# Optimization experiments

Measured on AMD Instinct MI355X. Metric: run time of the kernel, lower is better.

## Reference

```python
import jax, jax.numpy as jnp
import numpy as np

BS, SL, NN, NE = 8, 100, 200, 600
C = 110; CP1 = C + 1
D = 128          # node_embed_dim
DC = 64          # concept_embed_dim
H = 256          # lstm hidden
VOCAB = 50000
NPROB = 1000
FEAT = 2 + CP1 + DC  # LSTM input dim = 177


def setup_inputs() -> dict:
    key = jax.random.key(0)
    ks = jax.random.split(key, 24)
    f32 = jnp.float32
    p_id = jax.random.randint(ks[0], (BS, SL), 0, NPROB)
    c_id = jax.random.bernoulli(ks[1], 0.1, (BS, SL, CP1)).astype(f32)
    node_id = jax.random.randint(ks[2], (BS, SL, NN), 0, VOCAB)
    edge = jax.random.randint(ks[3], (BS, SL, 2, NE), 0, NN)
    edge_type = jax.random.randint(ks[4], (BS, SL, NE), 0, 8)
    target_c = jax.random.bernoulli(ks[5], 0.05, (BS, SL, CP1)).astype(f32)
    target_c = target_c.at[:, :, 0].set(1.0)  # every step has >=1 target concept
    result = jax.random.bernoulli(ks[6], 0.5, (BS * SL, 1)).astype(f32)
    c_embed = jax.random.bernoulli(ks[7], 0.1, (BS, SL, CP1)).astype(f32)
    cur_result = jax.random.normal(ks[8], (BS, SL, 2), f32)
    # parameters
    node_embed_w = jax.random.normal(ks[9], (VOCAB, D), f32) * 0.02
    edge_embed_w = (jax.random.normal(ks[10], (8, D), f32) * 0.02).at[0].set(0.0)  # padding_idx=0
    ggnn_w = jax.random.normal(ks[11], (4, D, D), f32) * 0.05
    gru_w_ih = jax.random.normal(ks[12], (3 * D, D), f32) * 0.05
    gru_w_hh = jax.random.normal(ks[13], (3 * D, D), f32) * 0.05
    gru_b_ih = jnp.zeros((3 * D,), f32)
    gru_b_hh = jnp.zeros((3 * D,), f32)
    transdim_w = jax.random.normal(ks[14], (DC, D), f32) * 0.05
    concept_embedding = jax.random.normal(ks[15], (CP1, DC), f32) * 0.05
    lstm_w_ih = jax.random.normal(ks[16], (4 * H, FEAT), f32) * 0.05
    lstm_w_hh = jax.random.normal(ks[17], (4 * H, H), f32) * 0.05
    lstm_b_ih = jnp.zeros((4 * H,), f32)
    lstm_b_hh = jnp.zeros((4 * H,), f32)
    pred_w = jax.random.normal(ks[18], (CP1, H), f32) * 0.05
    pred_b = jnp.zeros((CP1,), f32)
    return dict(p_id=p_id, c_id=c_id, node_id=node_id, edge=edge, edge_type=edge_type,
                target_c=target_c, result=result, c_embed=c_embed, cur_result=cur_result,
                node_embed_w=node_embed_w, edge_embed_w=edge_embed_w, ggnn_w=ggnn_w,
                gru_w_ih=gru_w_ih, gru_w_hh=gru_w_hh, gru_b_ih=gru_b_ih, gru_b_hh=gru_b_hh,
                transdim_w=transdim_w, concept_embedding=concept_embedding,
                lstm_w_ih=lstm_w_ih, lstm_w_hh=lstm_w_hh, lstm_b_ih=lstm_b_ih,
                lstm_b_hh=lstm_b_hh, pred_w=pred_w, pred_b=pred_b)


def _forward(p_id, c_id, node_id, edge, edge_type, target_c, result, c_embed, cur_result,
             node_embed_w, edge_embed_w, ggnn_w, gru_w_ih, gru_w_hh, gru_b_ih, gru_b_hh,
             transdim_w, concept_embedding, lstm_w_ih, lstm_w_hh, lstm_b_ih, lstm_b_hh,
             pred_w, pred_b):
    bs, sl = p_id.shape
    N = node_id.shape[2]
    G = bs * sl  # all graphs batched (replaces torch per-sample python loop)
    x = node_embed_w[node_id].reshape(G, N, -1)                       # [G,N,D]
    ew = edge_embed_w[edge_type].mean(-1).reshape(G, -1, 1)           # [G,E,1]
    e = edge.reshape(G, 2, -1)
    src, dst = e[:, 0], e[:, 1]                                       # [G,E]
    flat_dst = (dst + jnp.arange(G)[:, None] * N).reshape(-1)
    d = x.shape[-1]
    # GatedGraphConv, 4 layers: m = x @ W_l, sum-aggregate edge_weight*m[src] at dst, GRUCell update
    for l in range(4):
        m = jnp.einsum('gnd,de->gne', x, ggnn_w[l])
        gathered = jnp.take_along_axis(m, src[:, :, None], axis=1)    # [G,E,D]
        msg = (ew * gathered).reshape(-1, d)
        agg = jax.ops.segment_sum(msg, flat_dst, num_segments=G * N).reshape(G, N, d)
        gi = agg @ gru_w_ih.T + gru_b_ih
        gh = x @ gru_w_hh.T + gru_b_hh
        i_r, i_z, i_n = jnp.split(gi, 3, axis=-1)
        h_r, h_z, h_n = jnp.split(gh, 3, axis=-1)
        r = jax.nn.sigmoid(i_r + h_r)
        z = jax.nn.sigmoid(i_z + h_z)
        n = jnp.tanh(i_n + r * h_n)
        x = (1.0 - z) * n + z * x
    # transdim (node_embed_dim != concept_embed_dim)
    ggnn = jnp.einsum('gnd,cd->gnc', x, transdim_w)                   # [G,N,DC]
    # concept-node attention
    ce = c_embed.reshape(G, -1, 1)                                    # [G,C+1,1]
    query = ce * concept_embedding[None]                              # [G,C+1,DC]
    attn_w = jax.nn.softmax(jnp.einsum('gcd,gnd->gcn', query, ggnn), axis=2)
    attn = jnp.einsum('gcn,gnd->gcd', attn_w, ggnn) * ce
    num = jnp.sum(c_id, axis=2).reshape(G, 1)
    num = jnp.where(num == 0, 1.0, num)
    attn_out = (jnp.sum(attn, axis=1) / num).reshape(bs, sl, -1)
    # LSTM (1 layer, batch_first)
    lstm_in = jnp.concatenate([c_embed, attn_out, cur_result], axis=2)
    hdim = pred_w.shape[1]
    def step(carry, xt):
        h, c = carry
        gates = xt @ lstm_w_ih.T + lstm_b_ih + h @ lstm_w_hh.T + lstm_b_hh
        i, f, g, o = jnp.split(gates, 4, axis=-1)
        c = jax.nn.sigmoid(f) * c + jax.nn.sigmoid(i) * jnp.tanh(g)
        h = jax.nn.sigmoid(o) * jnp.tanh(c)
        return (h, c), h
    init = (jnp.zeros((bs, hdim), lstm_in.dtype), jnp.zeros((bs, hdim), lstm_in.dtype))
    _, hs = jax.lax.scan(step, init, jnp.swapaxes(lstm_in, 0, 1))
    lstm_out = jnp.swapaxes(hs, 0, 1).reshape(G, hdim)
    # prediction + masked BCE-with-logits
    pred = lstm_out @ pred_w.T + pred_b                               # [G,C+1]
    tc = target_c.reshape(G, -1)
    pred1 = jnp.sum(pred * tc, axis=1)
    nc = jnp.sum(tc, axis=1)
    mask = nc > 0
    fp = pred1 / jnp.where(mask, nc, 1.0)
    ft = result.reshape(-1)
    bce = jnp.maximum(fp, 0.0) - fp * ft + jnp.log1p(jnp.exp(-jnp.abs(fp)))
    mf = mask.astype(fp.dtype)
    loss = jnp.sum(bce * mf) / jnp.maximum(jnp.sum(mf), 1.0)
    return loss, jax.nn.sigmoid(fp), ft


def reference(p_id, c_id, node_id, edge, edge_type, target_c, result, c_embed, cur_result,
              node_embed_w, edge_embed_w, ggnn_w, gru_w_ih, gru_w_hh, gru_b_ih, gru_b_hh,
              transdim_w, concept_embedding, lstm_w_ih, lstm_w_hh, lstm_b_ih, lstm_b_hh,
              pred_w, pred_b):
    return _forward(p_id, c_id, node_id, edge, edge_type, target_c, result, c_embed, cur_result,
                    node_embed_w, edge_embed_w, ggnn_w, gru_w_ih, gru_w_hh, gru_b_ih, gru_b_hh,
                    transdim_w, concept_embedding, lstm_w_ih, lstm_w_hh, lstm_b_ih, lstm_b_hh,
                    pred_w, pred_b)
```

## Files before the change

### kernel.cpp

```cpp
#include <hip/hip_runtime.h>
#include <math.h>

static const int BSZ   = 8;
static const int SLN   = 100;
static const int NNODE = 200;
static const int NEDGE = 600;
static const int CP1N  = 111;
static const int DIM   = 128;
static const int DCN   = 64;
static const int HID   = 256;
static const int FEATN = 177;
static const int GN    = 800;
static const int MROW  = 160000;

typedef unsigned short u16;
typedef u16    u16x8  __attribute__((ext_vector_type(8)));
typedef __bf16 bf16x8 __attribute__((ext_vector_type(8)));
typedef __bf16 bf16x2 __attribute__((ext_vector_type(2)));
typedef float  f32x16 __attribute__((ext_vector_type(16)));

#if defined(__has_builtin)
# if __has_builtin(__builtin_amdgcn_fdot2_f32_bf16)
#  define HAVE_FDOT2 1
# else
// ... 103 lines not shown
    } else if (idx < 172032){
        int t = idx - 163840;
        twb[t] = f2bf(tw[t]);
    }
}

__global__ void __launch_bounds__(256)
k_build_csr(const int* __restrict__ edge, const int* __restrict__ etype,
            const float* __restrict__ eembed,
            int* __restrict__ csr_src, float* __restrict__ csr_w, int* __restrict__ csr_off){
    int g = blockIdx.x; int tid = threadIdx.x;
    __shared__ float tmean[8];
    __shared__ float tpart[8][32];
    __shared__ int cnt[NNODE];
    __shared__ int offs[NNODE+1];
    __shared__ int cur[NNODE];
    {
        int ty = tid >> 5, lane = tid & 31;
        float s = 0.f;
        for (int i = lane; i < DIM; i += 32) s += eembed[ty*DIM + i];
        tpart[ty][lane] = s;
    }
    for (int i = tid; i < NNODE; i += 256) cnt[i] = 0;
    __syncthreads();
    if (tid < 8){
        float s = 0.f;
        for (int i = 0; i < 32; i++) s += tpart[tid][i];
        tmean[tid] = s / (float)DIM;
    }
    for (int e = tid; e < NEDGE; e += 256){
        int dst = edge[((size_t)g*2+1)*NEDGE + e];
        atomicAdd(&cnt[dst], 1);
    }
    __syncthreads();
    if (tid == 0){
        int run = 0;
        for (int i = 0; i < NNODE; i++){ offs[i] = run; run += cnt[i]; }
        offs[NNODE] = run;
    }
    __syncthreads();
    for (int i = tid; i < NNODE; i += 256) cur[i] = offs[i];
    for (int i = tid; i < NNODE+1; i += 256) csr_off[(size_t)g*(NNODE+1)+i] = offs[i];
    __syncthreads();
    for (int e = tid; e < NEDGE; e += 256){
        int dst = edge[((size_t)g*2+1)*NEDGE + e];
        int src = edge[((size_t)g*2+0)*NEDGE + e];
        float w = tmean[etype[(size_t)g*NEDGE + e]];
        int pos = atomicAdd(&cur[dst], 1);
        csr_src[(size_t)g*NEDGE + pos] = src;
        csr_w [(size_t)g*NEDGE + pos] = w;
    }
}

__global__ void __launch_bounds__(256)
k_mm_scatter(const u16* __restrict__ xb, const u16* __restrict__ gwTb_l,
             const int* __restrict__ csr_src, const float* __restrict__ csr_w,
             const int* __restrict__ csr_off, u16* __restrict__ aggb,
             const float4* __restrict__ emb, const int* __restrict__ nid, int first){
    __shared__ u16 smem[224*128];
    __shared__ int   e_src[NEDGE];
    __shared__ float e_w[NEDGE];
    __shared__ int   offs_s[NNODE+1];
    int g = blockIdx.x;
    int tid = threadIdx.x;
    u16x8* afrag = (u16x8*)smem;
    if (first){
        for (int c = tid; c < 3584; c += 256){
            int row = c >> 4, kc8 = c & 15;
            u16x8 v = {};
            if (row < NNODE) v = pack_emb(emb, nid[(size_t)g*NNODE + row], kc8);
            afrag[afrag_slot(row, kc8)] = v;
        }
    } else {
        const u16x8* xg = (const u16x8*)(xb + (size_t)g*NNODE*DIM);
        for (int c = tid; c < 3584; c += 256){
            int row = c >> 4, kc8 = c & 15;
            u16x8 v = {};
            if (row < NNODE) v = xg[row*16 + kc8];
            afrag[afrag_slot(row, kc8)] = v;
        }
    }
    {
        const int*   srcp = csr_src + (size_t)g*NEDGE;
        const float* wp   = csr_w   + (size_t)g*NEDGE;
        const int*   off  = csr_off + (size_t)g*(NNODE+1);
        for (int i = tid; i < NEDGE; i += 256){ e_src[i] = srcp[i]; e_w[i] = wp[i]; }
        for (int i = tid; i <= NNODE; i += 256) offs_s[i] = off[i];
    }
    __syncthreads();
    int w = tid >> 6, lane = tid & 63;
    int nbase = w*32;
    int m = lane & 31, kh = lane >> 5;
    f32x16 acc[7];
    #pragma unroll
    for (int t = 0; t < 7; t++) acc[t] = (f32x16)0.f;
    const u16x8* bp = (const u16x8*)gwTb_l;
    int nrow = nbase + m;
    #pragma unroll
    for (int kc = 0; kc < 8; kc++){
        u16x8 b = bp[nrow*16 + kc*2 + kh];
        #pragma unroll
        for (int mt = 0; mt < 7; mt++){
            u16x8 a = afrag[(mt*8 + kc)*64 + (lane ^ kc)];
            acc[mt] = __builtin_amdgcn_mfma_f32_32x32x16_bf16(
                __builtin_bit_cast(bf16x8, a), __builtin_bit_cast(bf16x8, b), acc[mt], 0, 0, 0);
        }
    }
    __syncthreads();
    #pragma unroll
    for (int mt = 0; mt < 7; mt++){
        #pragma unroll
        for (int r = 0; r < 16; r++){
            int row = mt*32 + (r&3) + 8*(r>>2) + 4*kh;
            int col = nbase + m;
            smem[row*128 + col] = f2bf(acc[mt][r]);
        }
    }
    __syncthreads();
    const unsigned* m32 = (const unsigned*)smem;
    int j2 = tid & 63, rg = tid >> 6;
    unsigned* aggout = (unsigned*)(aggb + (size_t)g*NNODE*DIM);
    for (int i = 0; i < 50; i++){
        int n = rg*50 + i;
        int b0 = offs_s[n], e0 = offs_s[n+1];
        float a0 = 0.f, a1 = 0.f;
        for (int p = b0; p < e0; p++){
            unsigned mv = m32[e_src[p]*64 + j2];
            float w_ = e_w[p];
            a0 += w_ * bf2f((u16)(mv & 0xffffu));
            a1 += w_ * bf2f((u16)(mv >> 16));
        }
        aggout[(size_t)n*64 + j2] = (unsigned)f2bf(a0) | ((unsigned)f2bf(a1) << 16);
    }
}

__global__ void __launch_bounds__(512, 2)
k_gru_mfma(u16* __restrict__ xb, const u16* __restrict__ aggb,
           const u16* __restrict__ wihb, const u16* __restrict__ whhb,
           const float* __restrict__ bih, const float* __restrict__ bhh,
           const float4* __restrict__ emb, const int* __restrict__ nid, int first){
    __shared__ u16x8 afragA[2048];
    __shared__ u16x8 afragX[2048];
    int tid = threadIdx.x;
    long r0 = (long)blockIdx.x * 128;
    const u16x8* aggp = (const u16x8*)aggb;
    if (first){
        for (int c = tid; c < 2048; c += 512){
            int row = c >> 4, kc8 = c & 15;
            afragX[afrag_slot(row, kc8)] = pack_emb(emb, nid[r0 + row], kc8);
        }
        for (int c = tid; c < 2048; c += 512){
            int row = c >> 4, kc8 = c & 15;
            afragA[afrag_slot(row, kc8)] = aggp[(r0 + row)*16 + kc8];
        }
    } else {
        const u16x8* xbp = (const u16x8*)xb;
        for (int c = tid; c < 4096; c += 512){
            int mat = c >> 11, cc = c & 2047;
            int row = cc >> 4, kc8 = cc & 15;
            u16x8 v = (mat ? xbp : aggp)[(r0 + row)*16 + kc8];
            (mat ? afragX : afragA)[afrag_slot(row, kc8)] = v;
        }
    }
    __syncthreads();
    int w = tid >> 6, lane = tid & 63;
    int mtg = w >> 2;
    int cb  = (w & 3) * 32;
    f32x16 acc0[6], acc1[6];
    #pragma unroll
    for (int t = 0; t < 6; t++){ acc0[t] = (f32x16)0.f; acc1[t] = (f32x16)0.f; }
    const u16x8* bi = (const u16x8*)wihb;
    const u16x8* bh = (const u16x8*)whhb;
    int kh = lane >> 5;
    int ncol = cb + (lane & 31);
    #pragma unroll
    for (int kc = 0; kc < 8; kc++){
        int lx = lane ^ kc;
        u16x8 aA0 = afragA[((2*mtg+0)*8 + kc)*64 + lx];
        u16x8 aA1 = afragA[((2*mtg+1)*8 + kc)*64 + lx];
        u16x8 aX0 = afragX[((2*mtg+0)*8 + kc)*64 + lx];
        u16x8 aX1 = afragX[((2*mtg+1)*8 + kc)*64 + lx];
        #pragma unroll
        for (int g3 = 0; g3 < 3; g3++){
            int n = g3*128 + ncol;
            u16x8 b1 = bi[n*16 + kc*2 + kh];
            u16x8 b2 = bh[n*16 + kc*2 + kh];
            acc0[g3]   = __builtin_amdgcn_mfma_f32_32x32x16_bf16(
                __builtin_bit_cast(bf16x8, aA0), __builtin_bit_cast(bf16x8, b1), acc0[g3], 0,0,0);
            acc1[g3]   = __builtin_amdgcn_mfma_f32_32x32x16_bf16(
                __builtin_bit_cast(bf16x8, aA1), __builtin_bit_cast(bf16x8, b1), acc1[g3], 0,0,0);
            acc0[3+g3] = __builtin_amdgcn_mfma_f32_32x32x16_bf16(
                __builtin_bit_cast(bf16x8, aX0), __builtin_bit_cast(bf16x8, b2), acc0[3+g3], 0,0,0);
            acc1[3+g3] = __builtin_amdgcn_mfma_f32_32x32x16_bf16(
                __builtin_bit_cast(bf16x8, aX1), __builtin_bit_cast(bf16x8, b2), acc1[3+g3], 0,0,0);
        }
    }
    int col = cb + (lane & 31);
    float bir = bih[col], biz = bih[col+128], bin = bih[col+256];
    float bhr = bhh[col], bhz = bhh[col+128], bhn = bhh[col+256];
    int kc8c = col >> 3, elc = col & 7;
    #pragma unroll
    for (int mt2 = 0; mt2 < 2; mt2++){
        const f32x16* ac = mt2 ? acc1 : acc0;
        #pragma unroll
        for (int r = 0; r < 16; r++){
            int row = mtg*64 + mt2*32 + (r&3) + 8*(r>>2) + 4*kh;
            u16x8 xv = afragX[afrag_slot(row, kc8c)];
            float xo = bf2f(((const u16*)&xv)[elc]);
            float rr  = sigf(ac[0][r] + bir + ac[3][r] + bhr);
            float zz  = sigf(ac[1][r] + biz + ac[4][r] + bhz);
            float nn_ = tanh_f(ac[2][r] + bin + rr*(ac[5][r] + bhn));
            float xn  = (1.f - zz)*nn_ + zz*xo;
            xb[(size_t)(r0 + row)*DIM + col] = f2bf(xn);
        }
    }
}

__global__ void __launch_bounds__(256)
k_attention(const u16* __restrict__ xb, const u16* __restrict__ twb,
            const float* __restrict__ cemb, const float* __restrict__ cid,
            const float* __restrict__ conc, const float* __restrict__ curres,
            float* __restrict__ lstm_in){
    int g = blockIdx.x; int tid = threadIdx.x;
    int lane = tid & 63, wv = tid >> 6;
    __shared__ __align__(16) unsigned char smem_raw[57344];
    __shared__ float ce_s[CP1N];
    __shared__ float sc4[4][256];
    __shared__ float wredA[4][4];
    __shared__ float wredB[4][4];
    __shared__ float part4[4][4][DCN];
    __shared__ float oacc[DCN];
    __shared__ float num_s;
    __shared__ int actv[CP1N];
    __shared__ int nact_s;
    u16x8* afrag = (u16x8*)smem_raw;
    float* gg    = (float*)smem_raw;
    const u16x8* xg = (const u16x8*)(xb + (size_t)g*NNODE*DIM);
    for (int c = tid; c < 3584; c += 256){
        int row = c >> 4, kc8 = c & 15;
        u16x8 v = {};
        if (row < NNODE) v = xg[row*16 + kc8];
        afrag[afrag_slot(row, kc8)] = v;
    }
    if (tid == 0) nact_s = 0;
    if (tid < CP1N) ce_s[tid] = cemb[(size_t)g*CP1N + tid];
    if (tid < DCN) oacc[tid] = 0.f;
    {
        float v = (tid < CP1N) ? cid[(size_t)g*CP1N + tid] : 0.f;
        #pragma unroll
        for (int m2 = 32; m2; m2 >>= 1) v += __shfl_xor(v, m2);
        if (lane == 0) wredA[wv][0] = v;
    }
    __syncthreads();
    if (tid == 0){
        float nm = wredA[0][0]+wredA[1][0]+wredA[2][0]+wredA[3][0];
        num_s = (nm == 0.f) ? 1.f : nm;
    }
    if (tid < CP1N && ce_s[tid] != 0.f){
        int p = atomicAdd(&nact_s, 1);
        actv[p] = tid;
    }
    {
        int ct = wv & 1, rh = wv >> 1;
        int tb = rh ? 4 : 0;
        int ntile = rh ? 3 : 4;
        int m = lane & 31, kh = lane >> 5;
        f32x16 acc[4];
        #pragma unroll
        for (int t = 0; t < 4; t++) acc[t] = (f32x16)0.f;
        const u16x8* tp = (const u16x8*)twb;
        #pragma unroll
        for (int kc = 0; kc < 8; kc++){
            u16x8 b = tp[(ct*32 + m)*16 + kc*2 + kh];
            #pragma unroll
            for (int t = 0; t < 4; t++){
                if (t < ntile){
                    u16x8 a = afrag[((tb+t)*8 + kc)*64 + (lane ^ kc)];
                    acc[t] = __builtin_amdgcn_mfma_f32_32x32x16_bf16(
                        __builtin_bit_cast(bf16x8, a), __builtin_bit_cast(bf16x8, b), acc[t], 0,0,0);
                }
            }
        }
        __syncthreads();
        #pragma unroll
        for (int t = 0; t < 4; t++){
            if (t < ntile){
                #pragma unroll
                for (int r = 0; r < 16; r++){
                    int row = (tb+t)*32 + (r&3) + 8*(r>>2) + 4*kh;
                    int col = ct*32 + m;
                    if (row < NNODE) gg[row*65 + col] = acc[t][r];
                }
            }
        }
    }
    __syncthreads();
    int nact = nact_s;
    for (int ci = 0; ci < nact; ci += 4){
        int i0 = actv[ci];
        int i1 = actv[(ci+1 < nact) ? ci+1 : nact-1];
        int i2 = actv[(ci+2 < nact) ? ci+2 : nact-1];
        int i3 = actv[(ci+3 < nact) ? ci+3 : nact-1];
        float ce0 = ce_s[i0], ce1 = ce_s[i1], ce2 = ce_s[i2], ce3 = ce_s[i3];
        const float* q0 = conc + i0*DCN;
        const float* q1 = conc + i1*DCN;
        const float* q2 = conc + i2*DCN;
        const float* q3 = conc + i3*DCN;
        float s0=-1e30f, s1=-1e30f, s2=-1e30f, s3=-1e30f;
        if (tid < NNODE){
            float a0=0.f,a1=0.f,a2=0.f,a3=0.f;
            const float* gr_ = &gg[tid*65];
            #pragma unroll 8
            for (int d = 0; d < DCN; d++){
                float gv = gr_[d];
                a0 += q0[d]*gv; a1 += q1[d]*gv; a2 += q2[d]*gv; a3 += q3[d]*gv;
            }
            s0 = ce0*a0; s1 = ce1*a1; s2 = ce2*a2; s3 = ce3*a3;
        }
        float m0=s0, m1=s1, m2=s2, m3=s3;
        #pragma unroll
        for (int mk = 32; mk; mk >>= 1){
            m0 = fmaxf(m0, __shfl_xor(m0, mk));
            m1 = fmaxf(m1, __shfl_xor(m1, mk));
            m2 = fmaxf(m2, __shfl_xor(m2, mk));
            m3 = fmaxf(m3, __shfl_xor(m3, mk));
        }
        if (lane == 0){ wredA[wv][0]=m0; wredA[wv][1]=m1; wredA[wv][2]=m2; wredA[wv][3]=m3; }
        __syncthreads();
        float mx0 = fmaxf(fmaxf(wredA[0][0],wredA[1][0]), fmaxf(wredA[2][0],wredA[3][0]));
        float mx1 = fmaxf(fmaxf(wredA[0][1],wredA[1][1]), fmaxf(wredA[2][1],wredA[3][1]));
        float mx2 = fmaxf(fmaxf(wredA[0][2],wredA[1][2]), fmaxf(wredA[2][2],wredA[3][2]));
        float mx3 = fmaxf(fmaxf(wredA[0][3],wredA[1][3]), fmaxf(wredA[2][3],wredA[3][3]));
        float e0 = (tid < NNODE) ? fexp2(LOG2E*(s0-mx0)) : 0.f;
        float e1 = (tid < NNODE) ? fexp2(LOG2E*(s1-mx1)) : 0.f;
        float e2 = (tid < NNODE) ? fexp2(LOG2E*(s2-mx2)) : 0.f;
        float e3 = (tid < NNODE) ? fexp2(LOG2E*(s3-mx3)) : 0.f;
        sc4[0][tid]=e0; sc4[1][tid]=e1; sc4[2][tid]=e2; sc4[3][tid]=e3;
        float u0=e0,u1=e1,u2=e2,u3=e3;
        #pragma unroll
        for (int mk = 32; mk; mk >>= 1){
            u0 += __shfl_xor(u0, mk);
            u1 += __shfl_xor(u1, mk);
            u2 += __shfl_xor(u2, mk);
            u3 += __shfl_xor(u3, mk);
        }
        if (lane == 0){ wredB[wv][0]=u0; wredB[wv][1]=u1; wredB[wv][2]=u2; wredB[wv][3]=u3; }
        __syncthreads();
        float inv0 = ce0 / (wredB[0][0]+wredB[1][0]+wredB[2][0]+wredB[3][0]);
        float inv1 = (ci+1 < nact) ? ce1 / (wredB[0][1]+wredB[1][1]+wredB[2][1]+wredB[3][1]) : 0.f;
        float inv2 = (ci+2 < nact) ? ce2 / (wredB[0][2]+wredB[1][2]+wredB[2][2]+wredB[3][2]) : 0.f;
        float inv3 = (ci+3 < nact) ? ce3 / (wredB[0][3]+wredB[1][3]+wredB[2][3]+wredB[3][3]) : 0.f;
        float pa0=0.f, pa1=0.f, pa2=0.f, pa3=0.f;
        for (int n = wv; n < NNODE; n += 4){
            float gv = gg[n*65 + lane];
            pa0 += sc4[0][n]*gv; pa1 += sc4[1][n]*gv;
            pa2 += sc4[2][n]*gv; pa3 += sc4[3][n]*gv;
        }
        part4[wv][0][lane]=pa0; part4[wv][1][lane]=pa1;
        part4[wv][2][lane]=pa2; part4[wv][3][lane]=pa3;
        __syncthreads();
        if (tid < DCN){
            float t0 = part4[0][0][tid]+part4[1][0][tid]+part4[2][0][tid]+part4[3][0][tid];
            float t1 = part4[0][1][tid]+part4[1][1][tid]+part4[2][1][tid]+part4[3][1][tid];
            float t2 = part4[0][2][tid]+part4[1][2][tid]+part4[2][2][tid]+part4[3][2][tid];
            float t3 = part4[0][3][tid]+part4[1][3][tid]+part4[2][3][tid]+part4[3][3][tid];
            oacc[tid] += inv0*t0 + inv1*t1 + inv2*t2 + inv3*t3;
        }
    }
    __syncthreads();
    if (tid < FEATN){
        float v;
        if      (tid < CP1N)       v = ce_s[tid];
        else if (tid < CP1N+DCN)   v = oacc[tid-CP1N] / num_s;
        else                       v = curres[(size_t)g*2 + (tid-CP1N-DCN)];
        lstm_in[(size_t)g*FEATN + tid] = v;
    }
}

__global__ void __launch_bounds__(256)
k_gi(const float* __restrict__ lstm_in, const float* __restrict__ wihT,
     const float* __restrict__ bih, const float* __restrict__ bhh, float* __restrict__ gi){
    int rb = blockIdx.x;
    int jb = blockIdx.y;
    int tid = threadIdx.x;
    __shared__ float in_s[8][FEATN];
    for (int i = tid; i < 8*FEATN; i += 256){ int r = i/FEATN, k = i%FEATN; in_s[r][k] = lstm_in[((size_t)rb*8+r)*FEATN + k]; }
    __syncthreads();
    int j = jb*256 + tid;
    float acc[8];
    #pragma unroll
    for (int i = 0; i < 8; i++) acc[i] = 0.f;
    for (int k = 0; k < FEATN; k++){
        float w = wihT[(size_t)k*1024 + j];
        #pragma unroll
        for (int i = 0; i < 8; i++) acc[i] += in_s[i][k] * w;
    }
    float b = bih[j] + bhh[j];
    #pragma unroll
    for (int i = 0; i < 8; i++) gi[((size_t)rb*8+i)*1024 + j] = acc[i] + b;
}

static const int WREG = 104;
static const int WL4  = 6;

__global__ void __launch_bounds__(1024)
__attribute__((amdgpu_waves_per_eu(4,4)))
k_lstm(const float* __restrict__ gi, const unsigned* __restrict__ whhP, float* __restrict__ out){
    int b = blockIdx.x; int tid = threadIdx.x;
    __shared__ uint4 ldsw4[WL4][1024];
    __shared__ float gates[1024];
    __shared__ __align__(8) u16 h16[HID];
    unsigned wreg[WREG];
    #pragma unroll
    for (int i = 0; i < WREG; i++) wreg[i] = whhP[(size_t)i*1024 + tid];
    #pragma unroll
    for (int q = 0; q < WL4; q++){
        uint4 v;
        v.x = whhP[(size_t)(WREG + 4*q + 0)*1024 + tid];
        v.y = whhP[(size_t)(WREG + 4*q + 1)*1024 + tid];
        v.z = whhP[(size_t)(WREG + 4*q + 2)*1024 + tid];
        v.w = whhP[(size_t)(WREG + 4*q + 3)*1024 + tid];
        ldsw4[q][tid] = v;
    }
    if (tid < 128) ((unsigned*)h16)[tid] = 0u;
    float c_reg = 0.f;
    int lane = tid & 63;
    __syncthreads();
    float giv = gi[(size_t)b*SLN*1024 + tid];
// ... 75 lines not shown
        __syncthreads();
    }
    if (tid == 0){
        float nc = redn[0];
        bool mask = nc > 0.f;
        float fp = redv[0] / (mask ? nc : 1.f);
        float ft = result[row];
        float bce = fmaxf(fp, 0.f) - fp*ft + log1pf(expf(-fabsf(fp)));
        out[1 + row]      = 1.f/(1.f + expf(-fp));
        out[1 + GN + row] = ft;
        if (mask){ atomicAdd(&lacc[0], bce); atomicAdd(&lacc[1], 1.f); }
    }
}

__global__ void k_loss_final(const float* __restrict__ lacc, float* __restrict__ out){
    out[0] = lacc[0] / fmaxf(lacc[1], 1.f);
}

extern "C" void kernel_launch(void* const* d_in, const int* in_sizes, int n_in,
                              void* d_out, int out_size, void* d_ws, size_t ws_size,
                              hipStream_t stream) {
    const float* c_id        = (const float*)d_in[1];
    const int*   node_id     = (const int*)  d_in[2];
    const int*   edge        = (const int*)  d_in[3];
    const int*   etype       = (const int*)  d_in[4];
    const float* target_c    = (const float*)d_in[5];
    const float* result      = (const float*)d_in[6];
    const float* c_embed     = (const float*)d_in[7];
    const float* cur_result  = (const float*)d_in[8];
    const float* node_emb_w  = (const float*)d_in[9];
    const float* edge_emb_w  = (const float*)d_in[10];
    const float* ggnn_w      = (const float*)d_in[11];
    const float* gru_w_ih    = (const float*)d_in[12];
    const float* gru_w_hh    = (const float*)d_in[13];
    const float* gru_b_ih    = (const float*)d_in[14];
    const float* gru_b_hh    = (const float*)d_in[15];
    const float* transdim_w  = (const float*)d_in[16];
    const float* concept     = (const float*)d_in[17];
    const float* lstm_w_ih   = (const float*)d_in[18];
    const float* lstm_w_hh   = (const float*)d_in[19];
    const float* lstm_b_ih   = (const float*)d_in[20];
    const float* lstm_b_hh   = (const float*)d_in[21];
    const float* pred_w      = (const float*)d_in[22];
    const float* pred_b      = (const float*)d_in[23];
    float* out = (float*)d_out;

    char* ws = (char*)d_ws;
    size_t off = 0;
    auto alloc = [&](size_t bytes) -> void* {
        void* p = ws + off;
        off += (bytes + 255) & ~(size_t)255;
        return p;
    };
    u16*      xb       = (u16*)     alloc((size_t)MROW*DIM*2);
    u16*      aggb     = (u16*)     alloc((size_t)MROW*DIM*2);
    int*      csr_src  = (int*)     alloc((size_t)GN*NEDGE*4);
    float*    csr_w    = (float*)   alloc((size_t)GN*NEDGE*4);
    int*      csr_off  = (int*)     alloc((size_t)GN*(NNODE+1)*4);
    float*    lstm_in  = (float*)   alloc((size_t)GN*FEATN*4);
    float*    gi       = (float*)   alloc((size_t)GN*1024*4);
    unsigned* whhP     = (unsigned*)alloc((size_t)128*1024*4);
    float*    wihT     = (float*)   alloc((size_t)FEATN*1024*4);
    float*    lstm_out = (float*)   alloc((size_t)GN*HID*4);
    u16*      wihb     = (u16*)     alloc((size_t)384*128*2);
    u16*      whhb     = (u16*)     alloc((size_t)384*128*2);
    u16*      gwTb     = (u16*)     alloc((size_t)4*128*128*2);
    u16*      twb      = (u16*)     alloc((size_t)DCN*DIM*2);
    float*    lacc     = (float*)   alloc(256);

    hipMemsetAsync(lacc, 0, 8, stream);
    {
        int total = 128*1024 + FEATN*1024;
        k_transpose_w<<<(total + 255)/256, 256, 0, stream>>>(lstm_w_hh, lstm_w_ih, whhP, wihT);
    }
    k_convert_w<<<672, 256, 0, stream>>>(gru_w_ih, gru_w_hh, ggnn_w, transdim_w, wihb, whhb, gwTb, twb);
    k_build_csr<<<GN, 256, 0, stream>>>(edge, etype, edge_emb_w, csr_src, csr_w, csr_off);
    for (int l = 0; l < 4; l++){
        k_mm_scatter<<<GN, 256, 0, stream>>>(xb, gwTb + (size_t)l*DIM*DIM,
                                             csr_src, csr_w, csr_off, aggb,
                                             (const float4*)node_emb_w, node_id, l == 0);
        k_gru_mfma<<<MROW/128, 512, 0, stream>>>(xb, aggb, wihb, whhb, gru_b_ih, gru_b_hh,
                                                 (const float4*)node_emb_w, node_id, l == 0);
    }
    k_attention<<<GN, 256, 0, stream>>>(xb, twb, c_embed, c_id, concept, cur_result, lstm_in);
    k_gi<<<dim3(100, 4), 256, 0, stream>>>(lstm_in, wihT, lstm_b_ih, lstm_b_hh, gi);
    k_lstm<<<BSZ, 1024, 0, stream>>>(gi, whhP, lstm_out);
    k_final<<<GN, 128, 0, stream>>>(lstm_out, pred_w, pred_b, target_c, result, out, lacc);
    k_loss_final<<<1, 1, 0, stream>>>(lacc, out);
}
```

Measured before the change: 1.123 ms.

## Fuse all GGNN layers, GRU updates and attention into one per-graph kernel

Replaces the four pairs of message-matmul/scatter and GRU kernels plus the attention kernel with a single 512-thread kernel per graph. Node states and aggregated messages stay in LDS across all four layers, which removes the global xb/aggb round trips and eight kernel launches. The message matrix is built in two 64-column halves so it fits in scratch. In exchange, occupancy drops sharply because of the large LDS footprint, and the GRU GEMM now runs at only 800 blocks with some idle waves for the 7-tile split.

```diff
diff --git a/kernel.cpp b/kernel.cpp
--- a/kernel.cpp
+++ b/kernel.cpp
@@ -179,230 +179,183 @@
     }
 }
 
-__global__ void __launch_bounds__(256)
-k_mm_scatter(const u16* __restrict__ xb, const u16* __restrict__ gwTb_l,
-             const int* __restrict__ csr_src, const float* __restrict__ csr_w,
-             const int* __restrict__ csr_off, u16* __restrict__ aggb,
-             const float4* __restrict__ emb, const int* __restrict__ nid, int first){
-    __shared__ u16 smem[224*128];
+__global__ void __launch_bounds__(512)
+k_ggnn(const float4* __restrict__ emb, const int* __restrict__ nid,
+       const u16* __restrict__ gwTb, const u16* __restrict__ wihb,
+       const u16* __restrict__ whhb, const float* __restrict__ bih,
+       const float* __restrict__ bhh,
+       const int* __restrict__ csr_src, const float* __restrict__ csr_w,
+       const int* __restrict__ csr_off, const u16* __restrict__ twb,
+       const float* __restrict__ cemb, const float* __restrict__ cid,
+       const float* __restrict__ conc, const float* __restrict__ curres,
+       float* __restrict__ lstm_in){
+    __shared__ u16x8 Xf[3584];
+    __shared__ u16x8 Af[3584];
+    __shared__ __align__(16) unsigned char scratch[28672];
     __shared__ int   e_src[NEDGE];
     __shared__ float e_w[NEDGE];
     __shared__ int   offs_s[NNODE+1];
-    int g = blockIdx.x;
-    int tid = threadIdx.x;
-    u16x8* afrag = (u16x8*)smem;
-    if (first){
-        for (int c = tid; c < 3584; c += 256){
-            int row = c >> 4, kc8 = c & 15;
-            u16x8 v = {};
-            if (row < NNODE) v = pack_emb(emb, nid[(size_t)g*NNODE + row], kc8);
-            afrag[afrag_slot(row, kc8)] = v;
-        }
-    } else {
-        const u16x8* xg = (const u16x8*)(xb + (size_t)g*NNODE*DIM);
-        for (int c = tid; c < 3584; c += 256){
-            int row = c >> 4, kc8 = c & 15;
-            u16x8 v = {};
-            if (row < NNODE) v = xg[row*16 + kc8];
-            afrag[afrag_slot(row, kc8)] = v;
-        }
+    __shared__ float ce_s[CP1N];
+    __shared__ float redw[8];
+    __shared__ float num_s;
+    __shared__ int   actv[CP1N];
+    __shared__ int   nact_s;
+
+    int g = blockIdx.x; int tid = threadIdx.x;
+    int lane = tid & 63, wv = tid >> 6;
+    int m = lane & 31, kh = lane >> 5;
+
+    for (int c = tid; c < 3584; c += 512){
+        int row = c >> 4, kc8 = c & 15;
+        u16x8 v = {};
+        if (row < NNODE) v = pack_emb(emb, nid[(size_t)g*NNODE + row], kc8);
+        Xf[afrag_slot(row, kc8)] = v;
     }
     {
         const int*   srcp = csr_src + (size_t)g*NEDGE;
         const float* wp   = csr_w   + (size_t)g*NEDGE;
         const int*   off  = csr_off + (size_t)g*(NNODE+1);
-        for (int i = tid; i < NEDGE; i += 256){ e_src[i] = srcp[i]; e_w[i] = wp[i]; }
-        for (int i = tid; i <= NNODE; i += 256) offs_s[i] = off[i];
-    }
-    __syncthreads();
-    int w = tid >> 6, lane = tid & 63;
-    int nbase = w*32;
-    int m = lane & 31, kh = lane >> 5;
-    f32x16 acc[7];
-    #pragma unroll
-    for (int t = 0; t < 7; t++) acc[t] = (f32x16)0.f;
-    const u16x8* bp = (const u16x8*)gwTb_l;
-    int nrow = nbase + m;
-    #pragma unroll
-    for (int kc = 0; kc < 8; kc++){
-        u16x8 b = bp[nrow*16 + kc*2 + kh];
-        #pragma unroll
-        for (int mt = 0; mt < 7; mt++){
-            u16x8 a = afrag[(mt*8 + kc)*64 + (lane ^ kc)];
-            acc[mt] = __builtin_amdgcn_mfma_f32_32x32x16_bf16(
-                __builtin_bit_cast(bf16x8, a), __builtin_bit_cast(bf16x8, b), acc[mt], 0, 0, 0);
-        }
-    }
-    __syncthreads();
-    #pragma unroll
-    for (int mt = 0; mt < 7; mt++){
-        #pragma unroll
-        for (int r = 0; r < 16; r++){
-            int row = mt*32 + (r&3) + 8*(r>>2) + 4*kh;
-            int col = nbase + m;
-            smem[row*128 + col] = f2bf(acc[mt][r]);
-        }
-    }
-    __syncthreads();
-    const unsigned* m32 = (const unsigned*)smem;
-    int j2 = tid & 63, rg = tid >> 6;
-    unsigned* aggout = (unsigned*)(aggb + (size_t)g*NNODE*DIM);
-    for (int i = 0; i < 50; i++){
-        int n = rg*50 + i;
-        int b0 = offs_s[n], e0 = offs_s[n+1];
-        float a0 = 0.f, a1 = 0.f;
-        for (int p = b0; p < e0; p++){
-            unsigned mv = m32[e_src[p]*64 + j2];
-            float w_ = e_w[p];
-            a0 += w_ * bf2f((u16)(mv & 0xffffu));
-            a1 += w_ * bf2f((u16)(mv >> 16));
-        }
-        aggout[(size_t)n*64 + j2] = (unsigned)f2bf(a0) | ((unsigned)f2bf(a1) << 16);
-    }
-}
-
-__global__ void __launch_bounds__(512, 2)
-k_gru_mfma(u16* __restrict__ xb, const u16* __restrict__ aggb,
-           const u16* __restrict__ wihb, const u16* __restrict__ whhb,
-           const float* __restrict__ bih, const float* __restrict__ bhh,
-           const float4* __restrict__ emb, const int* __restrict__ nid, int first){
-    __shared__ u16x8 afragA[2048];
-    __shared__ u16x8 afragX[2048];
-    int tid = threadIdx.x;
-    long r0 = (long)blockIdx.x * 128;
-    const u16x8* aggp = (const u16x8*)aggb;
-    if (first){
-        for (int c = tid; c < 2048; c += 512){
-            int row = c >> 4, kc8 = c & 15;
-            afragX[afrag_slot(row, kc8)] = pack_emb(emb, nid[r0 + row], kc8);
-        }
-        for (int c = tid; c < 2048; c += 512){
-            int row = c >> 4, kc8 = c & 15;
-            afragA[afrag_slot(row, kc8)] = aggp[(r0 + row)*16 + kc8];
-        }
-    } else {
-        const u16x8* xbp = (const u16x8*)xb;
-        for (int c = tid; c < 4096; c += 512){
-            int mat = c >> 11, cc = c & 2047;
-            int row = cc >> 4, kc8 = cc & 15;
-            u16x8 v = (mat ? xbp : aggp)[(r0 + row)*16 + kc8];
-            (mat ? afragX : afragA)[afrag_slot(row, kc8)] = v;
-        }
-    }
-    __syncthreads();
-    int w = tid >> 6, lane = tid & 63;
-    int mtg = w >> 2;
-    int cb  = (w & 3) * 32;
-    f32x16 acc0[6], acc1[6];
-    #pragma unroll
-    for (int t = 0; t < 6; t++){ acc0[t] = (f32x16)0.f; acc1[t] = (f32x16)0.f; }
-    const u16x8* bi = (const u16x8*)wihb;
-    const u16x8* bh = (const u16x8*)whhb;
-    int kh = lane >> 5;
-    int ncol = cb + (lane & 31);
-    #pragma unroll
-    for (int kc = 0; kc < 8; kc++){
-        int lx = lane ^ kc;
-        u16x8 aA0 = afragA[((2*mtg+0)*8 + kc)*64 + lx];
-        u16x8 aA1 = afragA[((2*mtg+1)*8 + kc)*64 + lx];
-        u16x8 aX0 = afragX[((2*mtg+0)*8 + kc)*64 + lx];
-        u16x8 aX1 = afragX[((2*mtg+1)*8 + kc)*64 + lx];
-        #pragma unroll
-        for (int g3 = 0; g3 < 3; g3++){
-            int n = g3*128 + ncol;
-            u16x8 b1 = bi[n*16 + kc*2 + kh];
-            u16x8 b2 = bh[n*16 + kc*2 + kh];
-            acc0[g3]   = __builtin_amdgcn_mfma_f32_32x32x16_bf16(
-                __builtin_bit_cast(bf16x8, aA0), __builtin_bit_cast(bf16x8, b1), acc0[g3], 0,0,0);
-            acc1[g3]   = __builtin_amdgcn_mfma_f32_32x32x16_bf16(
-                __builtin_bit_cast(bf16x8, aA1), __builtin_bit_cast(bf16x8, b1), acc1[g3], 0,0,0);
-            acc0[3+g3] = __builtin_amdgcn_mfma_f32_32x32x16_bf16(
-                __builtin_bit_cast(bf16x8, aX0), __builtin_bit_cast(bf16x8, b2), acc0[3+g3], 0,0,0);
-            acc1[3+g3] = __builtin_amdgcn_mfma_f32_32x32x16_bf16(
-                __builtin_bit_cast(bf16x8, aX1), __builtin_bit_cast(bf16x8, b2), acc1[3+g3], 0,0,0);
-        }
-    }
-    int col = cb + (lane & 31);
-    float bir = bih[col], biz = bih[col+128], bin = bih[col+256];
-    float bhr = bhh[col], bhz = bhh[col+128], bhn = bhh[col+256];
-    int kc8c = col >> 3, elc = col & 7;
-    #pragma unroll
-    for (int mt2 = 0; mt2 < 2; mt2++){
-        const f32x16* ac = mt2 ? acc1 : acc0;
-        #pragma unroll
-        for (int r = 0; r < 16; r++){
-            int row = mtg*64 + mt2*32 + (r&3) + 8*(r>>2) + 4*kh;
-            u16x8 xv = afragX[afrag_slot(row, kc8c)];
-            float xo = bf2f(((const u16*)&xv)[elc]);
-            float rr  = sigf(ac[0][r] + bir + ac[3][r] + bhr);
-            float zz  = sigf(ac[1][r] + biz + ac[4][r] + bhz);
-            float nn_ = tanh_f(ac[2][r] + bin + rr*(ac[5][r] + bhn));
-            float xn  = (1.f - zz)*nn_ + zz*xo;
-            xb[(size_t)(r0 + row)*DIM + col] = f2bf(xn);
-        }
-    }
-}
-
-__global__ void __launch_bounds__(256)
-k_attention(const u16* __restrict__ xb, const u16* __restrict__ twb,
-            const float* __restrict__ cemb, const float* __restrict__ cid,
-            const float* __restrict__ conc, const float* __restrict__ curres,
-            float* __restrict__ lstm_in){
-    int g = blockIdx.x; int tid = threadIdx.x;
-    int lane = tid & 63, wv = tid >> 6;
-    __shared__ __align__(16) unsigned char smem_raw[57344];
-    __shared__ float ce_s[CP1N];
-    __shared__ float sc4[4][256];
-    __shared__ float wredA[4][4];
-    __shared__ float wredB[4][4];
-    __shared__ float part4[4][4][DCN];
-    __shared__ float oacc[DCN];
-    __shared__ float num_s;
-    __shared__ int actv[CP1N];
-    __shared__ int nact_s;
-    u16x8* afrag = (u16x8*)smem_raw;
-    float* gg    = (float*)smem_raw;
-    const u16x8* xg = (const u16x8*)(xb + (size_t)g*NNODE*DIM);
-    for (int c = tid; c < 3584; c += 256){
-        int row = c >> 4, kc8 = c & 15;
-        u16x8 v = {};
-        if (row < NNODE) v = xg[row*16 + kc8];
-        afrag[afrag_slot(row, kc8)] = v;
+        for (int i = tid; i < NEDGE; i += 512){ e_src[i] = srcp[i]; e_w[i] = wp[i]; }
+        for (int i = tid; i <= NNODE; i += 512) offs_s[i] = off[i];
     }
     if (tid == 0) nact_s = 0;
     if (tid < CP1N) ce_s[tid] = cemb[(size_t)g*CP1N + tid];
-    if (tid < DCN) oacc[tid] = 0.f;
     {
         float v = (tid < CP1N) ? cid[(size_t)g*CP1N + tid] : 0.f;
         #pragma unroll
         for (int m2 = 32; m2; m2 >>= 1) v += __shfl_xor(v, m2);
-        if (lane == 0) wredA[wv][0] = v;
+        if (lane == 0) redw[wv] = v;
     }
     __syncthreads();
     if (tid == 0){
-        float nm = wredA[0][0]+wredA[1][0]+wredA[2][0]+wredA[3][0];
+        float nm = 0.f;
+        for (int i = 0; i < 8; i++) nm += redw[i];
         num_s = (nm == 0.f) ? 1.f : nm;
     }
     if (tid < CP1N && ce_s[tid] != 0.f){
         int p = atomicAdd(&nact_s, 1);
         actv[p] = tid;
     }
+
+    for (int l = 0; l < 4; l++){
+        const u16x8* bp = (const u16x8*)(gwTb + (size_t)l*DIM*DIM);
+        for (int h = 0; h < 2; h++){
+            int ct  = wv & 1;
+            int rgm = wv >> 1;
+            int nbase = (2*h + ct)*32;
+            int nrow  = nbase + m;
+            f32x16 acc[2];
+            acc[0] = (f32x16)0.f; acc[1] = (f32x16)0.f;
+            #pragma unroll
+            for (int kc = 0; kc < 8; kc++){
+                u16x8 b = bp[nrow*16 + kc*2 + kh];
+                #pragma unroll
+                for (int t = 0; t < 2; t++){
+                    int mt = rgm*2 + t;
+                    if (mt < 7){
+                        u16x8 a = Xf[(mt*8 + kc)*64 + (lane ^ kc)];
+                        acc[t] = __builtin_amdgcn_mfma_f32_32x32x16_bf16(
+                            __builtin_bit_cast(bf16x8, a), __builtin_bit_cast(bf16x8, b), acc[t], 0,0,0);
+                    }
+                }
+            }
+            __syncthreads();
+            u16* m_s = (u16*)scratch;
+            #pragma unroll
+            for (int t = 0; t < 2; t++){
+                int mt = rgm*2 + t;
+                if (mt < 7){
+                    #pragma unroll
+                    for (int r = 0; r < 16; r++){
+                        int row = mt*32 + (r&3) + 8*(r>>2) + 4*kh;
+                        m_s[row*64 + ct*32 + m] = f2bf(acc[t][r]);
+                    }
+                }
+            }
+            __syncthreads();
+            const unsigned* m32 = (const unsigned*)scratch;
+            int j2 = tid & 31, rgrp = tid >> 5;
+            int kc8 = 8*h + (j2 >> 2);
+            for (int n = rgrp; n < NNODE; n += 16){
+                int b0 = offs_s[n], e0 = offs_s[n+1];
+                float a0 = 0.f, a1 = 0.f;
+                for (int p = b0; p < e0; p++){
+                    unsigned mv = m32[e_src[p]*32 + j2];
+                    float w_ = e_w[p];
+                    a0 += w_ * bf2f((u16)(mv & 0xffffu));
+                    a1 += w_ * bf2f((u16)(mv >> 16));
+                }
+                ((unsigned*)Af)[afrag_slot(n, kc8)*4 + (j2 & 3)] =
+                    (unsigned)f2bf(a0) | ((unsigned)f2bf(a1) << 16);
+            }
+            __syncthreads();
+        }
+        {
+            int cb  = (wv & 3)*32;
+            int grp = wv >> 2;
+            int col = cb + m;
+            float bir = bih[col], biz = bih[col+128], bin = bih[col+256];
+            float bhr = bhh[col], bhz = bhh[col+128], bhn = bhh[col+256];
+            int kc8c = col >> 3, elc = col & 7;
+            const u16x8* bi = (const u16x8*)wihb;
+            const u16x8* bh = (const u16x8*)whhb;
+            for (int it = 0; it < 4; it++){
+                int mt = grp + it*2;
+                bool active = (mt < 7);
+                f32x16 a6[6];
+                #pragma unroll
+                for (int t = 0; t < 6; t++) a6[t] = (f32x16)0.f;
+                if (active){
+                    #pragma unroll
+                    for (int kc = 0; kc < 8; kc++){
+                        int lx = lane ^ kc;
+                        u16x8 aA = Af[(mt*8 + kc)*64 + lx];
+                        u16x8 aX = Xf[(mt*8 + kc)*64 + lx];
+                        #pragma unroll
+                        for (int g3 = 0; g3 < 3; g3++){
+                            int n = g3*128 + col;
+                            u16x8 b1 = bi[n*16 + kc*2 + kh];
+                            u16x8 b2 = bh[n*16 + kc*2 + kh];
+                            a6[g3]   = __builtin_amdgcn_mfma_f32_32x32x16_bf16(
+                                __builtin_bit_cast(bf16x8, aA), __builtin_bit_cast(bf16x8, b1), a6[g3], 0,0,0);
+                            a6[3+g3] = __builtin_amdgcn_mfma_f32_32x32x16_bf16(
+                                __builtin_bit_cast(bf16x8, aX), __builtin_bit_cast(bf16x8, b2), a6[3+g3], 0,0,0);
+                        }
+                    }
+                }
+                __syncthreads();
+                if (active){
+                    #pragma unroll
+                    for (int r = 0; r < 16; r++){
+                        int row = mt*32 + (r&3) + 8*(r>>2) + 4*kh;
+                        int slot = afrag_slot(row, kc8c);
+                        float xo = bf2f(((const u16*)Xf)[slot*8 + elc]);
+                        float rr  = sigf(a6[0][r] + bir + a6[3][r] + bhr);
+                        float zz  = sigf(a6[1][r] + biz + a6[4][r] + bhz);
+                        float nn_ = tanh_f(a6[2][r] + bin + rr*(a6[5][r] + bhn));
+                        float xn  = (1.f - zz)*nn_ + zz*xo;
+                        ((u16*)Xf)[slot*8 + elc] = f2bf(xn);
+                    }
+                }
+                __syncthreads();
+            }
+        }
+    }
+
+    float* gg = (float*)Af;
     {
         int ct = wv & 1, rh = wv >> 1;
-        int tb = rh ? 4 : 0;
-        int ntile = rh ? 3 : 4;
-        int m = lane & 31, kh = lane >> 5;
-        f32x16 acc[4];
-        #pragma unroll
-        for (int t = 0; t < 4; t++) acc[t] = (f32x16)0.f;
         const u16x8* tp = (const u16x8*)twb;
+        f32x16 acc[2];
+        acc[0] = (f32x16)0.f; acc[1] = (f32x16)0.f;
         #pragma unroll
         for (int kc = 0; kc < 8; kc++){
             u16x8 b = tp[(ct*32 + m)*16 + kc*2 + kh];
             #pragma unroll
-            for (int t = 0; t < 4; t++){
-                if (t < ntile){
-                    u16x8 a = afrag[((tb+t)*8 + kc)*64 + (lane ^ kc)];
+            for (int t = 0; t < 2; t++){
+                int mt = rh*2 + t;
+                if (mt < 7){
+                    u16x8 a = Xf[(mt*8 + kc)*64 + (lane ^ kc)];
                     acc[t] = __builtin_amdgcn_mfma_f32_32x32x16_bf16(
                         __builtin_bit_cast(bf16x8, a), __builtin_bit_cast(bf16x8, b), acc[t], 0,0,0);
                 }
@@ -410,97 +363,117 @@
         }
         __syncthreads();
         #pragma unroll
-        for (int t = 0; t < 4; t++){
-            if (t < ntile){
+        for (int t = 0; t < 2; t++){
+            int mt = rh*2 + t;
+            if (mt < 7){
                 #pragma unroll
                 for (int r = 0; r < 16; r++){
-                    int row = (tb+t)*32 + (r&3) + 8*(r>>2) + 4*kh;
-                    int col = ct*32 + m;
-                    if (row < NNODE) gg[row*65 + col] = acc[t][r];
-                }
-            }
-        }
-    }
-    __syncthreads();
-    int nact = nact_s;
-    for (int ci = 0; ci < nact; ci += 4){
-        int i0 = actv[ci];
-        int i1 = actv[(ci+1 < nact) ? ci+1 : nact-1];
-        int i2 = actv[(ci+2 < nact) ? ci+2 : nact-1];
-        int i3 = actv[(ci+3 < nact) ? ci+3 : nact-1];
-        float ce0 = ce_s[i0], ce1 = ce_s[i1], ce2 = ce_s[i2], ce3 = ce_s[i3];
-        const float* q0 = conc + i0*DCN;
-        const float* q1 = conc + i1*DCN;
-        const float* q2 = conc + i2*DCN;
-        const float* q3 = conc + i3*DCN;
-        float s0=-1e30f, s1=-1e30f, s2=-1e30f, s3=-1e30f;
-        if (tid < NNODE){
-            float a0=0.f,a1=0.f,a2=0.f,a3=0.f;
-            const float* gr_ = &gg[tid*65];
-            #pragma unroll 8
-            for (int d = 0; d < DCN; d++){
-                float gv = gr_[d];
-                a0 += q0[d]*gv; a1 += q1[d]*gv; a2 += q2[d]*gv; a3 += q3[d]*gv;
-            }
-            s0 = ce0*a0; s1 = ce1*a1; s2 = ce2*a2; s3 = ce3*a3;
-        }
-        float m0=s0, m1=s1, m2=s2, m3=s3;
-        #pragma unroll
-        for (int mk = 32; mk; mk >>= 1){
-            m0 = fmaxf(m0, __shfl_xor(m0, mk));
-            m1 = fmaxf(m1, __shfl_xor(m1, mk));
-            m2 = fmaxf(m2, __shfl_xor(m2, mk));
-            m3 = fmaxf(m3, __shfl_xor(m3, mk));
-        }
-        if (lane == 0){ wredA[wv][0]=m0; wredA[wv][1]=m1; wredA[wv][2]=m2; wredA[wv][3]=m3; }
+                    int row = mt*32 + (r&3) + 8*(r>>2) + 4*kh;
+                    int colg = ct*32 + m;
+                    if (row < NNODE) gg[row*65 + colg] = acc[t][r];
+                }
+            }
+        }
+    }
+    __syncthreads();
+
+    {
+        float* sc0 = (float*)scratch;
+        float* part4 = sc0 + 4*224;
+        float* wredA = part4 + 8*4*64;
+        float* wredB = wredA + 32;
+        float* oacc  = wredB + 32;
+        if (tid < DCN) oacc[tid] = 0.f;
         __syncthreads();
-        float mx0 = fmaxf(fmaxf(wredA[0][0],wredA[1][0]), fmaxf(wredA[2][0],wredA[3][0]));
-        float mx1 = fmaxf(fmaxf(wredA[0][1],wredA[1][1]), fmaxf(wredA[2][1],wredA[3][1]));
-        float mx2 = fmaxf(fmaxf(wredA[0][2],wredA[1][2]), fmaxf(wredA[2][2],wredA[3][2]));
-        float mx3 = fmaxf(fmaxf(wredA[0][3],wredA[1][3]), fmaxf(wredA[2][3],wredA[3][3]));
-        float e0 = (tid < NNODE) ? fexp2(LOG2E*(s0-mx0)) : 0.f;
-        float e1 = (tid < NNODE) ? fexp2(LOG2E*(s1-mx1)) : 0.f;
-        float e2 = (tid < NNODE) ? fexp2(LOG2E*(s2-mx2)) : 0.f;
-        float e3 = (tid < NNODE) ? fexp2(LOG2E*(s3-mx3)) : 0.f;
-        sc4[0][tid]=e0; sc4[1][tid]=e1; sc4[2][tid]=e2; sc4[3][tid]=e3;
-        float u0=e0,u1=e1,u2=e2,u3=e3;
-        #pragma unroll
-        for (int mk = 32; mk; mk >>= 1){
-            u0 += __shfl_xor(u0, mk);
-            u1 += __shfl_xor(u1, mk);
-            u2 += __shfl_xor(u2, mk);
-            u3 += __shfl_xor(u3, mk);
-        }
-        if (lane == 0){ wredB[wv][0]=u0; wredB[wv][1]=u1; wredB[wv][2]=u2; wredB[wv][3]=u3; }
-        __syncthreads();
-        float inv0 = ce0 / (wredB[0][0]+wredB[1][0]+wredB[2][0]+wredB[3][0]);
-        float inv1 = (ci+1 < nact) ? ce1 / (wredB[0][1]+wredB[1][1]+wredB[2][1]+wredB[3][1]) : 0.f;
-        float inv2 = (ci+2 < nact) ? ce2 / (wredB[0][2]+wredB[1][2]+wredB[2][2]+wredB[3][2]) : 0.f;
-        float inv3 = (ci+3 < nact) ? ce3 / (wredB[0][3]+wredB[1][3]+wredB[2][3]+wredB[3][3]) : 0.f;
-        float pa0=0.f, pa1=0.f, pa2=0.f, pa3=0.f;
-        for (int n = wv; n < NNODE; n += 4){
-            float gv = gg[n*65 + lane];
-            pa0 += sc4[0][n]*gv; pa1 += sc4[1][n]*gv;
-            pa2 += sc4[2][n]*gv; pa3 += sc4[3][n]*gv;
-        }
-        part4[wv][0][lane]=pa0; part4[wv][1][lane]=pa1;
-        part4[wv][2][lane]=pa2; part4[wv][3][lane]=pa3;
-        __syncthreads();
-        if (tid < DCN){
-            float t0 = part4[0][0][tid]+part4[1][0][tid]+part4[2][0][tid]+part4[3][0][tid];
-            float t1 = part4[0][1][tid]+part4[1][1][tid]+part4[2][1][tid]+part4[3][1][tid];
-            float t2 = part4[0][2][tid]+part4[1][2][tid]+part4[2][2][tid]+part4[3][2][tid];
-            float t3 = part4[0][3][tid]+part4[1][3][tid]+part4[2][3][tid]+part4[3][3][tid];
-            oacc[tid] += inv0*t0 + inv1*t1 + inv2*t2 + inv3*t3;
-        }
-    }
-    __syncthreads();
-    if (tid < FEATN){
-        float v;
-        if      (tid < CP1N)       v = ce_s[tid];
-        else if (tid < CP1N+DCN)   v = oacc[tid-CP1N] / num_s;
-        else                       v = curres[(size_t)g*2 + (tid-CP1N-DCN)];
-        lstm_in[(size_t)g*FEATN + tid] = v;
+        int nact = nact_s;
+        for (int ci = 0; ci < nact; ci += 4){
+            int i0 = actv[ci];
+            int i1 = actv[(ci+1 < nact) ? ci+1 : nact-1];
+            int i2 = actv[(ci+2 < nact) ? ci+2 : nact-1];
+            int i3 = actv[(ci+3 < nact) ? ci+3 : nact-1];
+            float ce0 = ce_s[i0], ce1 = ce_s[i1], ce2 = ce_s[i2], ce3 = ce_s[i3];
+            const float* q0 = conc + i0*DCN;
+            const float* q1 = conc + i1*DCN;
+            const float* q2 = conc + i2*DCN;
+            const float* q3 = conc + i3*DCN;
+            float s0=-1e30f, s1=-1e30f, s2=-1e30f, s3=-1e30f;
+            if (tid < NNODE){
+                float a0=0.f,a1=0.f,a2=0.f,a3=0.f;
+                const float* gr_ = &gg[tid*65];
+                #pragma unroll 8
+                for (int d = 0; d < DCN; d++){
+                    float gv = gr_[d];
+                    a0 += q0[d]*gv; a1 += q1[d]*gv; a2 += q2[d]*gv; a3 += q3[d]*gv;
+                }
+                s0 = ce0*a0; s1 = ce1*a1; s2 = ce2*a2; s3 = ce3*a3;
+            }
+            float m0=s0, m1=s1, m2=s2, m3=s3;
+            #pragma unroll
+            for (int mk = 32; mk; mk >>= 1){
+                m0 = fmaxf(m0, __shfl_xor(m0, mk));
+                m1 = fmaxf(m1, __shfl_xor(m1, mk));
+                m2 = fmaxf(m2, __shfl_xor(m2, mk));
+                m3 = fmaxf(m3, __shfl_xor(m3, mk));
+            }
+            if (lane == 0){ wredA[wv*4+0]=m0; wredA[wv*4+1]=m1; wredA[wv*4+2]=m2; wredA[wv*4+3]=m3; }
+            __syncthreads();
+            float mx0=-1e30f, mx1=-1e30f, mx2=-1e30f, mx3=-1e30f;
+            #pragma unroll
+            for (int i = 0; i < 8; i++){
+                mx0 = fmaxf(mx0, wredA[i*4+0]); mx1 = fmaxf(mx1, wredA[i*4+1]);
+                mx2 = fmaxf(mx2, wredA[i*4+2]); mx3 = fmaxf(mx3, wredA[i*4+3]);
+            }
+            float e0 = (tid < NNODE) ? fexp2(LOG2E*(s0-mx0)) : 0.f;
+            float e1 = (tid < NNODE) ? fexp2(LOG2E*(s1-mx1)) : 0.f;
+            float e2 = (tid < NNODE) ? fexp2(LOG2E*(s2-mx2)) : 0.f;
+            float e3 = (tid < NNODE) ? fexp2(LOG2E*(s3-mx3)) : 0.f;
+            if (tid < 224){ sc0[0*224+tid]=e0; sc0[1*224+tid]=e1; sc0[2*224+tid]=e2; sc0[3*224+tid]=e3; }
+            float u0=e0,u1=e1,u2=e2,u3=e3;
+            #pragma unroll
+            for (int mk = 32; mk; mk >>= 1){
+                u0 += __shfl_xor(u0, mk);
+                u1 += __shfl_xor(u1, mk);
+                u2 += __shfl_xor(u2, mk);
+                u3 += __shfl_xor(u3, mk);
+            }
+            if (lane == 0){ wredB[wv*4+0]=u0; wredB[wv*4+1]=u1; wredB[wv*4+2]=u2; wredB[wv*4+3]=u3; }
+            __syncthreads();
+            float d0=0.f,d1=0.f,d2=0.f,d3=0.f;
+            #pragma unroll
+            for (int i = 0; i < 8; i++){
+                d0 += wredB[i*4+0]; d1 += wredB[i*4+1]; d2 += wredB[i*4+2]; d3 += wredB[i*4+3];
+            }
+            float inv0 = ce0 / d0;
+            float inv1 = (ci+1 < nact) ? ce1 / d1 : 0.f;
+            float inv2 = (ci+2 < nact) ? ce2 / d2 : 0.f;
+            float inv3 = (ci+3 < nact) ? ce3 / d3 : 0.f;
+            float pa0=0.f, pa1=0.f, pa2=0.f, pa3=0.f;
+            for (int n = wv; n < NNODE; n += 8){
+                float gv = gg[n*65 + lane];
+                pa0 += sc0[0*224+n]*gv; pa1 += sc0[1*224+n]*gv;
+                pa2 += sc0[2*224+n]*gv; pa3 += sc0[3*224+n]*gv;
+            }
+            part4[(wv*4+0)*64+lane]=pa0; part4[(wv*4+1)*64+lane]=pa1;
+            part4[(wv*4+2)*64+lane]=pa2; part4[(wv*4+3)*64+lane]=pa3;
+            __syncthreads();
+            if (tid < DCN){
+                float t0=0.f,t1=0.f,t2=0.f,t3=0.f;
+                #pragma unroll
+                for (int i = 0; i < 8; i++){
+                    t0 += part4[(i*4+0)*64+tid]; t1 += part4[(i*4+1)*64+tid];
+                    t2 += part4[(i*4+2)*64+tid]; t3 += part4[(i*4+3)*64+tid];
+                }
+                oacc[tid] += inv0*t0 + inv1*t1 + inv2*t2 + inv3*t3;
+            }
+            __syncthreads();
+        }
+        if (tid < FEATN){
+            float v;
+            if      (tid < CP1N)       v = ce_s[tid];
+            else if (tid < CP1N+DCN)   v = oacc[tid-CP1N] / num_s;
+            else                       v = curres[(size_t)g*2 + (tid-CP1N-DCN)];
+            lstm_in[(size_t)g*FEATN + tid] = v;
+        }
     }
 }
 
@@ -682,8 +655,6 @@
         off += (bytes + 255) & ~(size_t)255;
         return p;
     };
-    u16*      xb       = (u16*)     alloc((size_t)MROW*DIM*2);
-    u16*      aggb     = (u16*)     alloc((size_t)MROW*DIM*2);
     int*      csr_src  = (int*)     alloc((size_t)GN*NEDGE*4);
     float*    csr_w    = (float*)   alloc((size_t)GN*NEDGE*4);
     int*      csr_off  = (int*)     alloc((size_t)GN*(NNODE+1)*4);
@@ -705,14 +676,9 @@
     }
     k_convert_w<<<672, 256, 0, stream>>>(gru_w_ih, gru_w_hh, ggnn_w, transdim_w, wihb, whhb, gwTb, twb);
     k_build_csr<<<GN, 256, 0, stream>>>(edge, etype, edge_emb_w, csr_src, csr_w, csr_off);
-    for (int l = 0; l < 4; l++){
-        k_mm_scatter<<<GN, 256, 0, stream>>>(xb, gwTb + (size_t)l*DIM*DIM,
-                                             csr_src, csr_w, csr_off, aggb,
-                                             (const float4*)node_emb_w, node_id, l == 0);
-        k_gru_mfma<<<MROW/128, 512, 0, stream>>>(xb, aggb, wihb, whhb, gru_b_ih, gru_b_hh,
-                                                 (const float4*)node_emb_w, node_id, l == 0);
-    }
-    k_attention<<<GN, 256, 0, stream>>>(xb, twb, c_embed, c_id, concept, cur_result, lstm_in);
+    k_ggnn<<<GN, 512, 0, stream>>>((const float4*)node_emb_w, node_id, gwTb, wihb, whhb,
+                                   gru_b_ih, gru_b_hh, csr_src, csr_w, csr_off, twb,
+                                   c_embed, c_id, concept, cur_result, lstm_in);
     k_gi<<<dim3(100, 4), 256, 0, stream>>>(lstm_in, wihT, lstm_b_ih, lstm_b_hh, gi);
     k_lstm<<<BSZ, 1024, 0, stream>>>(gi, whhP, lstm_out);
     k_final<<<GN, 128, 0, stream>>>(lstm_out, pred_w, pred_b, target_c, result, out, lacc);
```

After: 1.507 ms. +34.1%, slower.
